# Performance work log

Hardware: AMD Instinct MI355X
Metric: run time of the kernel (lower is better)

## Reference

```python
import jax, jax.numpy as jnp
import numpy as np


def _others_idx(n):
    # idx[i] = all agent indices except i, in order (prev agents then next agents),
    # matching the torch cat([prev_agents_msgs, next_agents_msgs]) ordering.
    return np.array([[j for j in range(n) if j != i] for i in range(n)], dtype=np.int32)


def setup_inputs() -> dict:
    key = jax.random.key(0)
    ks = jax.random.split(key, 6)
    bs, T, n, msg_len, obs_dim, hidden = 64, 256, 8, 16, 128, 64
    in_dim = obs_dim + (n - 1) * msg_len  # 240
    return {
        "obs": jax.random.normal(ks[0], (bs, T, n, obs_dim), jnp.float32),
        "messages": jax.random.normal(ks[1], (bs, T, n, msg_len), jnp.float32),
        "W1": jax.random.normal(ks[2], (n, in_dim, hidden), jnp.float32) * 0.05,
        "b1": jax.random.normal(ks[3], (n, hidden), jnp.float32) * 0.05,
        "W2": jax.random.normal(ks[4], (n, hidden, 1), jnp.float32) * 0.05,
        "b2": jax.random.normal(ks[5], (n, 1), jnp.float32) * 0.05,
    }


def reference(obs, messages, W1, b1, W2, b2):
    bs, T, n, msg_len = messages.shape
    idx = jnp.asarray(_others_idx(n))  # [n, n-1]
    # For each agent i at time t>0: concat of all OTHER agents' messages at t-1.
    m_prev = messages[:, :-1]                      # [bs, T-1, n, msg_len]
    gathered = m_prev[:, :, idx]                   # [bs, T-1, n, n-1, msg_len]
    msgs = gathered.reshape(bs, T - 1, n, (n - 1) * msg_len)
    pad = jnp.zeros((bs, 1, n, (n - 1) * msg_len), msgs.dtype)  # t=0 has no prior msgs
    msgs = jnp.concatenate([pad, msgs], axis=1)    # [bs, T, n, (n-1)*msg_len]
    inputs = jnp.concatenate([obs, msgs], axis=3)  # [bs, T, n, in_dim]
    # Per-agent independent MLP critic: Linear -> ReLU -> Linear
    h = jax.nn.relu(jnp.einsum('btai,aih->btah', inputs, W1) + b1)
    q = jnp.einsum('btah,aho->btao', h, W2) + b2   # [bs, T, n, 1]
    return q
```

## Files before the change

kernel.cpp:

```cpp
#include <hip/hip_runtime.h>


#define NAGENTS 8
#define MSG_LEN 16
#define OBS_DIM 128
#define HIDDEN  64
#define IN_DIM  240
#define TT      256
#define ROWS    16384
#define KSTEPS  15
#define MTILE   256
#define NFRAG   (KSTEPS * 2 * 64 * 8)

typedef __attribute__((ext_vector_type(8)))  short bf16x8;
typedef __attribute__((ext_vector_type(16))) float f32x16;

__device__ __forceinline__ unsigned short f2bf(float x) {
    unsigned u = __float_as_uint(x);
    u += 0x7fffu + ((u >> 16) & 1u);
    return (unsigned short)(u >> 16);
}
__device__ __forceinline__ float bf2f(unsigned short h) {
    return __uint_as_float(((unsigned)h) << 16);
}

__global__ __launch_bounds__(512, 4) void accritic_mfma_kernel(
    const float* __restrict__ obs,
    const float* __restrict__ msgs,
    const float* __restrict__ W1,
    const float* __restrict__ b1,
    const float* __restrict__ W2,
    const float* __restrict__ b2,
    float* __restrict__ out)
{
    __shared__ unsigned short WH[NFRAG];
    __shared__ unsigned short WL[NFRAG];

    const int a   = blockIdx.y;
    const int tid = threadIdx.x;
    const float* __restrict__ w1a = W1 + (size_t)a * IN_DIM * HIDDEN;

#pragma unroll
    for (int i = 0; i < NFRAG / 512; ++i) {
        int e    = tid + i * 512;
        int j    = e & 7;
        int lane = (e >> 3) & 63;
        int nt   = (e >> 9) & 1;
        int ks   = e >> 10;
        int k    = ks * 16 + (lane >> 5) * 8 + j;
        int col  = nt * 32 + (lane & 31);
        float w  = w1a[k * HIDDEN + col];
        unsigned short h = f2bf(w);
        WH[e] = h;
        WL[e] = f2bf(w - bf2f(h));
    }
    __syncthreads();

    const int wv   = tid >> 6;
    const int lane = tid & 63;
    const int rl   = lane & 31;
    const int kg   = lane >> 5;
    const int r    = blockIdx.x * MTILE + wv * 32 + rl;
    const int t    = r & (TT - 1);
    const bool zmsg = (t == 0);
    const int  rs   = zmsg ? r : r - 1;

    const float* __restrict__ obsp = obs + ((size_t)r * NAGENTS + a) * OBS_DIM + kg * 8;
    const float* __restrict__ msgp = msgs + (size_t)rs * NAGENTS * MSG_LEN + kg * 8;

    f32x16 acc0, acc1;
#pragma unroll
    for (int i = 0; i < 16; ++i) { acc0[i] = 0.f; acc1[i] = 0.f; }

    const bf16x8* __restrict__ WH8 = reinterpret_cast<const bf16x8*>(WH);
    const bf16x8* __restrict__ WL8 = reinterpret_cast<const bf16x8*>(WL);

#pragma unroll
    for (int ks = 0; ks < KSTEPS; ++ks) {
        float4 f0, f1;
        if (ks < 8) {
            const float4* p = reinterpret_cast<const float4*>(obsp + ks * 16);
            f0 = p[0]; f1 = p[1];
        } else {
            int pidx = ks - 8;
            int jsrc = (pidx < a) ? pidx : pidx + 1;
            const float4* p = reinterpret_cast<const float4*>(msgp + jsrc * MSG_LEN);
            f0 = p[0]; f1 = p[1];
            if (zmsg) { f0 = make_float4(0.f, 0.f, 0.f, 0.f); f1 = f0; }
        }

        float xf[8] = { f0.x, f0.y, f0.z, f0.w, f1.x, f1.y, f1.z, f1.w };
        bf16x8 ahi, alo;
#pragma unroll
        for (int q = 0; q < 8; ++q) {
            unsigned short h = f2bf(xf[q]);
            ahi[q] = (short)h;
            alo[q] = (short)f2bf(xf[q] - bf2f(h));
        }

        bf16x8 bh0 = WH8[(ks * 2 + 0) * 64 + lane];
        bf16x8 bh1 = WH8[(ks * 2 + 1) * 64 + lane];
        bf16x8 bl0 = WL8[(ks * 2 + 0) * 64 + lane];
        bf16x8 bl1 = WL8[(ks * 2 + 1) * 64 + lane];

        acc0 = __builtin_amdgcn_mfma_f32_32x32x16_bf16(ahi, bh0, acc0, 0, 0, 0);
        acc1 = __builtin_amdgcn_mfma_f32_32x32x16_bf16(ahi, bh1, acc1, 0, 0, 0);
        acc0 = __builtin_amdgcn_mfma_f32_32x32x16_bf16(alo, bh0, acc0, 0, 0, 0);
        acc1 = __builtin_amdgcn_mfma_f32_32x32x16_bf16(alo, bh1, acc1, 0, 0, 0);
        acc0 = __builtin_amdgcn_mfma_f32_32x32x16_bf16(ahi, bl0, acc0, 0, 0, 0);
        acc1 = __builtin_amdgcn_mfma_f32_32x32x16_bf16(ahi, bl1, acc1, 0, 0, 0);
    }

    const int cl = lane & 31;
    const float b1v0 = b1[a * HIDDEN + cl];
    const float b1v1 = b1[a * HIDDEN + 32 + cl];
    const float w2v0 = W2[a * HIDDEN + cl];
    const float w2v1 = W2[a * HIDDEN + 32 + cl];
    const float b2v  = b2[a];

    float v[16];
#pragma unroll
    for (int i = 0; i < 16; ++i) {
        float h0 = fmaxf(acc0[i] + b1v0, 0.f);
        float h1 = fmaxf(acc1[i] + b1v1, 0.f);
        v[i] = h0 * w2v0 + h1 * w2v1;
    }
#pragma unroll
    for (int off = 16; off >= 1; off >>= 1) {
#pragma unroll
        for (int i = 0; i < 16; ++i) v[i] += __shfl_xor(v[i], off, 64);
    }

    if (cl == 0) {
        const int r0 = blockIdx.x * MTILE + wv * 32;
#pragma unroll
        for (int i = 0; i < 16; ++i) {
            int row = (i & 3) + 8 * (i >> 2) + 4 * kg;
            out[(size_t)(r0 + row) * NAGENTS + a] = v[i] + b2v;
        }
    }
}

extern "C" void kernel_launch(void* const* d_in, const int* in_sizes, int n_in,
                              void* d_out, int out_size, void* d_ws, size_t ws_size,
                              hipStream_t stream) {
    const float* obs  = (const float*)d_in[0];
    const float* msgs = (const float*)d_in[1];
    const float* W1   = (const float*)d_in[2];
    const float* b1   = (const float*)d_in[3];
    const float* W2   = (const float*)d_in[4];
    const float* b2   = (const float*)d_in[5];
    float* out = (float*)d_out;

    dim3 grid(ROWS / MTILE, NAGENTS);
    accritic_mfma_kernel<<<grid, dim3(512), 0, stream>>>(obs, msgs, W1, b1, W2, b2, out);
}
```

Before: 125.0 us.

## Preload all activations into registers and truncate high bf16 split

Issues all 30 float4 activation loads for obs and messages up front into registers before the MFMA loop, so memory latency overlaps instead of being exposed once per k-step. Weight staging now loads all W1 values into registers before converting them. The hi part of the bf16 split now uses truncation, which saves ALU work while the lo part still carries the residual. Occupancy launch bounds drop from 4 to 2 blocks per CU to make room for the extra registers, which lowers the wave count available to hide latency.

```diff
diff --git a/kernel.cpp b/kernel.cpp
--- a/kernel.cpp
+++ b/kernel.cpp
@@ -15,16 +15,13 @@
 typedef __attribute__((ext_vector_type(8)))  short bf16x8;
 typedef __attribute__((ext_vector_type(16))) float f32x16;
 
-__device__ __forceinline__ unsigned short f2bf(float x) {
+__device__ __forceinline__ unsigned short f2bf_rne(float x) {
     unsigned u = __float_as_uint(x);
     u += 0x7fffu + ((u >> 16) & 1u);
     return (unsigned short)(u >> 16);
 }
-__device__ __forceinline__ float bf2f(unsigned short h) {
-    return __uint_as_float(((unsigned)h) << 16);
-}
 
-__global__ __launch_bounds__(512, 4) void accritic_mfma_kernel(
+__global__ __launch_bounds__(512, 2) void accritic_mfma_kernel(
     const float* __restrict__ obs,
     const float* __restrict__ msgs,
     const float* __restrict__ W1,
@@ -40,19 +37,27 @@
     const int tid = threadIdx.x;
     const float* __restrict__ w1a = W1 + (size_t)a * IN_DIM * HIDDEN;
 
+    {
+        float wreg[NFRAG / 512];
 #pragma unroll
-    for (int i = 0; i < NFRAG / 512; ++i) {
-        int e    = tid + i * 512;
-        int j    = e & 7;
-        int lane = (e >> 3) & 63;
-        int nt   = (e >> 9) & 1;
-        int ks   = e >> 10;
-        int k    = ks * 16 + (lane >> 5) * 8 + j;
-        int col  = nt * 32 + (lane & 31);
-        float w  = w1a[k * HIDDEN + col];
-        unsigned short h = f2bf(w);
-        WH[e] = h;
-        WL[e] = f2bf(w - bf2f(h));
+        for (int i = 0; i < NFRAG / 512; ++i) {
+            int e    = tid + i * 512;
+            int j    = e & 7;
+            int lane = (e >> 3) & 63;
+            int nt   = (e >> 9) & 1;
+            int ks   = e >> 10;
+            int k    = ks * 16 + (lane >> 5) * 8 + j;
+            int col  = nt * 32 + (lane & 31);
+            wreg[i]  = w1a[k * HIDDEN + col];
+        }
+#pragma unroll
+        for (int i = 0; i < NFRAG / 512; ++i) {
+            int e = tid + i * 512;
+            unsigned u = __float_as_uint(wreg[i]);
+            float hif  = __uint_as_float(u & 0xffff0000u);
+            WH[e] = (unsigned short)(u >> 16);
+            WL[e] = f2bf_rne(wreg[i] - hif);
+        }
     }
     __syncthreads();
 
@@ -65,8 +70,28 @@
     const bool zmsg = (t == 0);
     const int  rs   = zmsg ? r : r - 1;
 
-    const float* __restrict__ obsp = obs + ((size_t)r * NAGENTS + a) * OBS_DIM + kg * 8;
-    const float* __restrict__ msgp = msgs + (size_t)rs * NAGENTS * MSG_LEN + kg * 8;
+    const float4* __restrict__ ob4 =
+        reinterpret_cast<const float4*>(obs + ((size_t)r * NAGENTS + a) * OBS_DIM + kg * 8);
+    const float4* __restrict__ mg4 =
+        reinterpret_cast<const float4*>(msgs + (size_t)rs * NAGENTS * MSG_LEN + kg * 8);
+
+    float4 ox[16];
+#pragma unroll
+    for (int ks = 0; ks < 8; ++ks) {
+        ox[2 * ks]     = ob4[ks * 4];
+        ox[2 * ks + 1] = ob4[ks * 4 + 1];
+    }
+    float4 mx[14];
+#pragma unroll
+    for (int p = 0; p < 7; ++p) {
+        int jsrc = (p < a) ? p : p + 1;
+        mx[2 * p]     = mg4[jsrc * 4];
+        mx[2 * p + 1] = mg4[jsrc * 4 + 1];
+    }
+    if (zmsg) {
+#pragma unroll
+        for (int i = 0; i < 14; ++i) mx[i] = make_float4(0.f, 0.f, 0.f, 0.f);
+    }
 
     f32x16 acc0, acc1;
 #pragma unroll
@@ -78,24 +103,17 @@
 #pragma unroll
     for (int ks = 0; ks < KSTEPS; ++ks) {
         float4 f0, f1;
-        if (ks < 8) {
-            const float4* p = reinterpret_cast<const float4*>(obsp + ks * 16);
-            f0 = p[0]; f1 = p[1];
-        } else {
-            int pidx = ks - 8;
-            int jsrc = (pidx < a) ? pidx : pidx + 1;
-            const float4* p = reinterpret_cast<const float4*>(msgp + jsrc * MSG_LEN);
-            f0 = p[0]; f1 = p[1];
-            if (zmsg) { f0 = make_float4(0.f, 0.f, 0.f, 0.f); f1 = f0; }
-        }
+        if (ks < 8) { f0 = ox[2 * ks];       f1 = ox[2 * ks + 1]; }
+        else        { f0 = mx[2 * (ks - 8)]; f1 = mx[2 * (ks - 8) + 1]; }
 
         float xf[8] = { f0.x, f0.y, f0.z, f0.w, f1.x, f1.y, f1.z, f1.w };
         bf16x8 ahi, alo;
 #pragma unroll
         for (int q = 0; q < 8; ++q) {
-            unsigned short h = f2bf(xf[q]);
-            ahi[q] = (short)h;
-            alo[q] = (short)f2bf(xf[q] - bf2f(h));
+            unsigned u = __float_as_uint(xf[q]);
+            float hif  = __uint_as_float(u & 0xffff0000u);
+            ahi[q] = (short)(u >> 16);
+            alo[q] = (short)f2bf_rne(xf[q] - hif);
         }
 
         bf16x8 bh0 = WH8[(ks * 2 + 0) * 64 + lane];
```

After: 121.6 us. 1.03x faster.
